# Optimization experiments

Hardware: AMD Instinct MI355X
Metric: run time of the kernel (lower is better)

The kernel has to match this reference:

```python
import jax, jax.numpy as jnp
import numpy as np
from jax import lax

# Static model/config sizes
B, ANG, C, H, NF, NB = 1, 9, 3, 128, 16, 2


def get_freq_position(n):
    """Anti-diagonal frequency bands of an n x n angular-DCT grid (python/static)."""
    bands = []
    for i in range(n):
        bands.append(([i], [0]))
    for j in range(1, n):
        bands.append(([n - 1], [j]))
    for item in bands:
        while item[0][0] > 0 and item[1][0] < n - 1:
            item[0].insert(0, item[0][0] - 1)
            item[1].insert(0, item[1][0] + 1)
    return bands


def dct_mat(n):
    """Orthonormal DCT-II matrix (row k = k-th basis)."""
    k = jnp.arange(n, dtype=jnp.float32)[:, None]
    i = jnp.arange(n, dtype=jnp.float32)[None, :]
    m = jnp.cos(jnp.pi * (i + 0.5) * k / n) * jnp.sqrt(2.0 / n)
    return m.at[0].multiply(1.0 / np.sqrt(2.0))


def conv3d(x, w, b):
    # x: (N, Cin, D, H, W), w: (Cout, Cin, 3, 3, 3)
    y = lax.conv_general_dilated(x, w, (1, 1, 1), 'SAME',
                                 dimension_numbers=('NCDHW', 'OIDHW', 'NCDHW'))
    return y + b[None, :, None, None, None]


def branch(cut, wi, bi, a, wb, bb):
    """init conv + NB ResBlock3D (PReLU -> Conv3d, residual), plus outer skip."""
    y0 = conv3d(cut, wi, bi)
    y = y0
    for k in range(NB):
        r = jnp.where(y >= 0, y, a[k] * y)  # PReLU (single-parameter)
        y = y + conv3d(r, wb[k], bb[k])
    return y0 + y


def setup_inputs() -> dict:
    key = jax.random.key(0)
    ks = jax.random.split(key, 32)

    def nrm(k, shape, s=0.05):
        return jax.random.normal(k, shape, dtype=jnp.float32) * s

    inp = {"x": jax.random.normal(ks[0], (B, ANG, ANG, C, H, H), dtype=jnp.float32)}
    i = 1
    for n in ("dc", "lo", "mi", "hi"):
        inp[f"w_{n}_i"] = nrm(ks[i], (NF, C, 3, 3, 3)); i += 1
        inp[f"b_{n}_i"] = nrm(ks[i], (NF,)); i += 1
        inp[f"a_{n}"] = jnp.full((NB,), 0.25, dtype=jnp.float32)
        inp[f"w_{n}"] = nrm(ks[i], (NB, NF, NF, 3, 3, 3)); i += 1
        inp[f"b_{n}"] = nrm(ks[i], (NB, NF)); i += 1
    inp["w_last"] = nrm(ks[i], (C, NF))  # 1x1 Conv2d, no bias
    return inp


def reference(x, w_dc_i, b_dc_i, a_dc, w_dc, b_dc,
              w_lo_i, b_lo_i, a_lo, w_lo, b_lo,
              w_mi_i, b_mi_i, a_mi, w_mi, b_mi,
              w_hi_i, b_hi_i, a_hi, w_hi, b_hi, w_last):
    b, u, v, c, h, w = x.shape
    Da = dct_mat(u)  # angular DCT (u == v)
    Ds = dct_mat(h)  # spatial DCT (h == w)

    # SpaAngDCT: spatial 2D DCT then angular 2D DCT
    xf = jnp.einsum('buvchw,Hh,Ww->buvcHW', x, Ds, Ds)
    xf = jnp.einsum('buvchw,Uu,Vv->bUVchw', xf, Da, Da)

    x_rec = jnp.zeros((b, NF, u, v, h, w), dtype=x.dtype)
    for idx, (ui, vi) in enumerate(get_freq_position(u)):
        if idx == 0:
            p = (w_dc_i, b_dc_i, a_dc, w_dc, b_dc)
        elif idx <= 2:
            p = (w_lo_i, b_lo_i, a_lo, w_lo, b_lo)
        elif idx <= u - 1:
            p = (w_mi_i, b_mi_i, a_mi, w_mi, b_mi)
        else:
            p = (w_hi_i, b_hi_i, a_hi, w_hi, b_hi)
        ua, va = jnp.array(ui), jnp.array(vi)
        cut = xf[:, ua, va].transpose(0, 2, 1, 3, 4)  # (b, c, L, h, w)
        out = branch(cut, *p)                          # (b, NF, L, h, w)
        x_rec = x_rec.at[:, :, ua, va].set(out)        # scatter band back

    # 'b c u v h w -> b c (u h) (v w)' then 1x1 conv (NF -> 3)
    xr = x_rec.transpose(0, 1, 2, 4, 3, 5).reshape(b, NF, u * h, v * w)
    xr = jnp.einsum('bnHW,on->boHW', xr, w_last)
    xr = xr.reshape(b, c, u, h, v, w).transpose(0, 2, 4, 1, 3, 5)  # (b,u,v,c,h,w)

    # InverseSpaAngDCT: angular IDCT then spatial IDCT
    xr = jnp.einsum('bUVchw,Uu,Vv->buvchw', xr, Da, Da)
    xr = jnp.einsum('buvcHW,Hh,Ww->buvchw', xr, Ds, Ds)
    return xr + x
```

## Files before the change

### kernel.cpp

```cpp
#include <hip/hip_runtime.h>
#include <hip/hip_bf16.h>
#include <math.h>

typedef __hip_bfloat16 bf16;
typedef __attribute__((ext_vector_type(8))) short short8;
typedef __attribute__((ext_vector_type(4))) float floatx4;
typedef __attribute__((ext_vector_type(4))) unsigned int uint4v;
typedef __attribute__((ext_vector_type(2))) unsigned int uint2v;

#define HW 16384
#define NSLICE 243

__constant__ int c_s_of_p[81] = {
  0, 1,1, 2,2,2, 3,3,3,3, 4,4,4,4,4, 5,5,5,5,5,5, 6,6,6,6,6,6,6,
  7,7,7,7,7,7,7,7, 8,8,8,8,8,8,8,8,8, 9,9,9,9,9,9,9,9,
  10,10,10,10,10,10,10, 11,11,11,11,11,11, 12,12,12,12,12,
  13,13,13,13, 14,14,14, 15,15, 16};
__constant__ int c_l_of_p[81] = {
  0, 0,1, 0,1,2, 0,1,2,3, 0,1,2,3,4, 0,1,2,3,4,5, 0,1,2,3,4,5,6,
  0,1,2,3,4,5,6,7, 0,1,2,3,4,5,6,7,8, 0,1,2,3,4,5,6,7,
  0,1,2,3,4,5,6, 0,1,2,3,4,5, 0,1,2,3,4, 0,1,2,3, 0,1,2, 0,1, 0};
__constant__ int c_L_of_s[17] = {1,2,3,4,5,6,7,8,9,8,7,6,5,4,3,2,1};
__constant__ int c_g_of_s[17] = {0,1,1,2,2,2,2,2,2,3,3,3,3,3,3,3,3};
__constant__ int c_pos_uv[81] = {
  0,1,3,6,10,15,21,28,36,
  2,4,7,11,16,22,29,37,45,
  5,8,12,17,23,30,38,46,53,
  9,13,18,24,31,39,47,54,60,
  14,19,25,32,40,48,55,61,66,
  20,26,33,41,49,56,62,67,71,
  27,34,42,50,57,63,68,72,75,
  35,43,51,58,64,69,73,76,78,
  44,52,59,65,70,74,77,79,80};

struct WPtrs {
  const float* wi[4]; const float* bi[4]; const float* a[4];
  const float* wb[4]; const float* bb[4]; const float* wl;
};

__device__ __forceinline__ unsigned short f2bf(float f) {
  return __bfloat16_as_ushort(__float2bfloat16(f));
}
__device__ __forceinline__ float bflo(unsigned int w) {
  return __uint_as_float(w << 16);
}
__device__ __forceinline__ float bfhi(unsigned int w) {
  return __uint_as_float(w & 0xffff0000u);
}
__device__ __forceinline__ unsigned int pack2(float a, float b) {
  return (unsigned int)f2bf(a) | ((unsigned int)f2bf(b) << 16);
}
__device__ __forceinline__ float invprelu(float v, float invA) {
  return (v >= 0.f) ? v : v * invA;
}
__device__ __forceinline__ void bfsplit(float v, unsigned short& hi, unsigned short& lo) {
  unsigned int bits = __float_as_uint(v);
  hi = (unsigned short)(bits >> 16);
  lo = f2bf(v - __uint_as_float(bits & 0xffff0000u));
}

__global__ __launch_bounds__(256) void k_setup(float* DaF,
                                               unsigned short* TFhi, unsigned short* TFlo,
                                               unsigned short* TIhi, unsigned short* TIlo) {
  const double PI = 3.14159265358979323846;
  int t = blockIdx.x * 256 + threadIdx.x;
  if (t < 81) {
    int U = t / 9, u = t % 9;
    double d = cos(PI * (u + 0.5) * U / 9.0) * sqrt(2.0 / 9.0);
    if (U == 0) d *= (1.0 / sqrt(2.0));
    DaF[t] = (float)d;
  }
  if (t < 16384) {
    int jj = t & 7, lane = (t >> 3) & 63, ks = (t >> 9) & 3, tile = t >> 11;
    int row = tile * 16 + (lane & 15);
    int colk = ks * 32 + (lane >> 4) * 8 + jj;
    double vF = cos(PI * (colk + 0.5) * row / 128.0) * sqrt(2.0 / 128.0);
    if (row == 0) vF *= (1.0 / sqrt(2.0));
    double vI = cos(PI * (row + 0.5) * colk / 128.0) * sqrt(2.0 / 128.0);
    if (colk == 0) vI *= (1.0 / sqrt(2.0));
    unsigned short h, l;
    bfsplit((float)vF, h, l); TFhi[t] = h; TFlo[t] = l;
    bfsplit((float)vI, h, l); TIhi[t] = h; TIlo[t] = l;
  }
}

__global__ __launch_bounds__(256) void k_prep(WPtrs P, unsigned short* Wmf,
                                              float* BiF, float* BbF,
                                              float* AF, float* WlF) {
  int t = blockIdx.x * 256 + threadIdx.x;
  if (t < 92160) {
    int s = t / 7680, r = t % 7680;
    int step = r / 512, r2 = r % 512;
    int lane = r2 >> 3, j = r2 & 7;
    int d = step / 5, i = step % 5;
    int q = lane >> 4, m = lane & 15;
    int tl = 2 * i + (q >> 1);
    int cin = (q & 1) * 8 + j;
    float val = 0.f;
    if (tl <= 8) {
      int ky = tl / 3, kx = tl % 3;
      int tap = d * 9 + ky * 3 + kx;
      if (s < 4) {
        if (cin < 3) val = P.wi[s][(m * 3 + cin) * 27 + tap];
      } else {
        int g = (s - 4) >> 1, k = (s - 4) & 1;
        val = P.wb[g][((k * 16 + m) * 16 + cin) * 27 + tap];
      }
    }
    Wmf[t] = f2bf(val);
  }
  if (t < 64)  BiF[t] = P.bi[t / 16][t % 16];
  if (t < 128) BbF[t] = P.bb[t / 32][t % 32];
  if (t < 8)   AF[t]  = P.a[t / 2][t % 2];
  if (t < 48)  WlF[t] = P.wl[t];
}

__global__ __launch_bounds__(256) void k_dct2(const float* __restrict__ X,
                                              const unsigned short* __restrict__ tabhi,
                                              const unsigned short* __restrict__ tablo,
                                              const float* __restrict__ xres,
                                              float* __restrict__ Y) {
  __shared__ unsigned short sThi[128 * 136];
  __shared__ unsigned short sTlo[128 * 136];
  int s = blockIdx.x;
  int t = threadIdx.x;
  int lane = t & 63, wv = t >> 6;
  int q = lane >> 4, n16 = lane & 15;
  const float* Xs = X + (size_t)s * HW;

  floatx4 acc[2][8];
#pragma unroll
  for (int mt = 0; mt < 2; mt++)
#pragma unroll
    for (int nt = 0; nt < 8; nt++) acc[mt][nt] = (floatx4){0.f, 0.f, 0.f, 0.f};

#pragma unroll
  for (int ks = 0; ks < 4; ks++) {
    short8 ahi[2], alo[2];
#pragma unroll
    for (int mt = 0; mt < 2; mt++) {
      const float* xp = Xs + (wv * 32 + mt * 16 + n16) * 128 + ks * 32 + q * 8;
      float4 a = *(const float4*)xp;
      float4 b = *(const float4*)(xp + 4);
      union { short8 v; unsigned short u[8]; } H, L;
      float xv[8] = {a.x, a.y, a.z, a.w, b.x, b.y, b.z, b.w};
#pragma unroll
      for (int j = 0; j < 8; j++) bfsplit(xv[j], H.u[j], L.u[j]);
      ahi[mt] = H.v; alo[mt] = L.v;
    }
#pragma unroll
    for (int nt = 0; nt < 8; nt++) {
      int e = nt * 2048 + ks * 512 + lane * 8;
      short8 bh = *(const short8*)(tabhi + e);
      short8 bl = *(const short8*)(tablo + e);
#pragma unroll
      for (int mt = 0; mt < 2; mt++) {
        acc[mt][nt] = __builtin_amdgcn_mfma_f32_16x16x32_bf16(ahi[mt], bl, acc[mt][nt], 0, 0, 0);
        acc[mt][nt] = __builtin_amdgcn_mfma_f32_16x16x32_bf16(alo[mt], bh, acc[mt][nt], 0, 0, 0);
        acc[mt][nt] = __builtin_amdgcn_mfma_f32_16x16x32_bf16(ahi[mt], bh, acc[mt][nt], 0, 0, 0);
      }
    }
  }

#pragma unroll
  for (int mt = 0; mt < 2; mt++)
#pragma unroll
    for (int nt = 0; nt < 8; nt++) {
      int col = nt * 16 + n16;
      int rowb = wv * 32 + mt * 16 + q * 4;
#pragma unroll
      for (int rp = 0; rp < 4; rp += 2) {
        unsigned short h0, l0, h1, l1;
        bfsplit(acc[mt][nt][rp], h0, l0);
        bfsplit(acc[mt][nt][rp + 1], h1, l1);
        int widx = (col * 136 + rowb + rp) >> 1;
        ((unsigned int*)sThi)[widx] = (unsigned int)h0 | ((unsigned int)h1 << 16);
        ((unsigned int*)sTlo)[widx] = (unsigned int)l0 | ((unsigned int)l1 << 16);
      }
    }
  __syncthreads();

#pragma unroll
  for (int mt = 0; mt < 2; mt++)
#pragma unroll
    for (int nt = 0; nt < 8; nt++) acc[mt][nt] = (floatx4){0.f, 0.f, 0.f, 0.f};

#pragma unroll
  for (int ks = 0; ks < 4; ks++) {
    short8 ahi[2], alo[2];
#pragma unroll
    for (int mt = 0; mt < 2; mt++) {
      int e = (wv * 2 + mt) * 2048 + ks * 512 + lane * 8;
      ahi[mt] = *(const short8*)(tabhi + e);
      alo[mt] = *(const short8*)(tablo + e);
    }
#pragma unroll
    for (int nt = 0; nt < 8; nt++) {
      int off = (nt * 16 + n16) * 136 + ks * 32 + q * 8;
      short8 bh = *(const short8*)(sThi + off);
      short8 bl = *(const short8*)(sTlo + off);
#pragma unroll
      for (int mt = 0; mt < 2; mt++) {
        acc[mt][nt] = __builtin_amdgcn_mfma_f32_16x16x32_bf16(ahi[mt], bl, acc[mt][nt], 0, 0, 0);
        acc[mt][nt] = __builtin_amdgcn_mfma_f32_16x16x32_bf16(alo[mt], bh, acc[mt][nt], 0, 0, 0);
        acc[mt][nt] = __builtin_amdgcn_mfma_f32_16x16x32_bf16(ahi[mt], bh, acc[mt][nt], 0, 0, 0);
      }
    }
  }

#pragma unroll
  for (int mt = 0; mt < 2; mt++)
#pragma unroll
    for (int nt = 0; nt < 8; nt++) {
      int row0 = wv * 32 + mt * 16 + q * 4;
      int col = nt * 16 + n16;
#pragma unroll
      for (int r = 0; r < 4; r++) {
        size_t oi = (size_t)s * HW + (size_t)(row0 + r) * 128 + col;
        float v = acc[mt][nt][r];
        if (xres) v += xres[oi];
        Y[oi] = v;
      }
    }
}

__global__ __launch_bounds__(256) void k_angu(const float* __restrict__ in,
                                              const float* __restrict__ DaF,
                                              float* __restrict__ out) {
  __shared__ float sDa[81];
  int t = threadIdx.x;
  if (t < 81) sDa[t] = DaF[t];
  __syncthreads();
  int idx = blockIdx.x * 256 + t;
  int hw = idx & (HW - 1);
  int r = idx >> 14;
  int c = r % 3, v = r / 3;
  float f[9];
#pragma unroll
  for (int u = 0; u < 9; u++) f[u] = in[(size_t)((u * 9 + v) * 3 + c) * HW + hw];
#pragma unroll
  for (int U = 0; U < 9; U++) {
    float acc = 0.f;
#pragma unroll
    for (int u = 0; u < 9; u++) acc += sDa[U * 9 + u] * f[u];
    out[(size_t)((U * 9 + v) * 3 + c) * HW + hw] = acc;
  }
}

__global__ __launch_bounds__(256) void k_angv(const float* __restrict__ in,
                                              const float* __restrict__ DaF,
                                              unsigned short* __restrict__ xf2b) {
  __shared__ float sDa[81];
  int t = threadIdx.x;
  if (t < 81) sDa[t] = DaF[t];
  __syncthreads();
  int idx = blockIdx.x * 256 + t;
  int hw = idx & (HW - 1);
  int r = idx >> 14;
  int c = r % 3, U = r / 3;
  float f[9];
#pragma unroll
  for (int v = 0; v < 9; v++) f[v] = in[(size_t)((U * 9 + v) * 3 + c) * HW + hw];
#pragma unroll
  for (int V = 0; V < 9; V++) {
    float acc = 0.f;
#pragma unroll
    for (int v = 0; v < 9; v++) acc += sDa[V * 9 + v] * f[v];
    size_t base = ((size_t)c_pos_uv[U * 9 + V] * HW + hw) * 4;
    xf2b[base + c] = f2bf(acc);
    if (c == 0) xf2b[base + 3] = 0;
  }
}

__global__ __launch_bounds__(256) void k_angvi(const float* __restrict__ xrb,
                                               const float* __restrict__ DaF,
                                               float* __restrict__ out) {
  __shared__ float sDa[81];
  int t = threadIdx.x;
  if (t < 81) sDa[t] = DaF[t];
  __syncthreads();
  int idx = blockIdx.x * 256 + t;
  int hw = idx & (HW - 1);
  int r = idx >> 14;
  int c = r % 3, U = r / 3;
  float f[9];
#pragma unroll
  for (int V = 0; V < 9; V++)
    f[V] = xrb[((size_t)c_pos_uv[U * 9 + V] * 3 + c) * HW + hw];
#pragma unroll
  for (int v = 0; v < 9; v++) {
    float acc = 0.f;
#pragma unroll
    for (int V = 0; V < 9; V++) acc += sDa[V * 9 + v] * f[V];
    out[(size_t)((U * 9 + v) * 3 + c) * HW + hw] = acc;
  }
}

__global__ __launch_bounds__(256) void k_angui(const float* __restrict__ in,
                                               const float* __restrict__ DaF,
                                               float* __restrict__ out) {
  __shared__ float sDa[81];
  int t = threadIdx.x;
  if (t < 81) sDa[t] = DaF[t];
  __syncthreads();
  int idx = blockIdx.x * 256 + t;
  int hw = idx & (HW - 1);
  int r = idx >> 14;
  int c = r % 3, v = r / 3;
  float f[9];
#pragma unroll
  for (int U = 0; U < 9; U++) f[U] = in[(size_t)((U * 9 + v) * 3 + c) * HW + hw];
#pragma unroll
  for (int u = 0; u < 9; u++) {
    float acc = 0.f;
#pragma unroll
    for (int U = 0; U < 9; U++) acc += sDa[U * 9 + u] * f[U];
    out[(size_t)((u * 9 + v) * 3 + c) * HW + hw] = acc;
  }
}

__global__ __launch_bounds__(256) void k_conv(const unsigned short* __restrict__ src,
                                              const unsigned short* __restrict__ prevAct,
                                              const unsigned short* __restrict__ Wmf,
                                              const float* __restrict__ BiF,
                                              const float* __restrict__ BbF,
                                              const float* __restrict__ AF,
                                              int sel,
                                              unsigned short* __restrict__ bout) {
  __shared__ unsigned short s_lds[12672];
  int p = blockIdx.y;
  int s = c_s_of_p[p], l = c_l_of_p[p];
  int g = c_g_of_s[s], Ls = c_L_of_s[s];
  int row0 = blockIdx.x * 4;
  int t = threadIdx.x;
  int lane = t & 63, wv = t >> 6;
  int q = lane >> 4, n = lane & 15;

  float aNext = (sel < 2) ? AF[g * 2 + sel] : 0.f;
  float invA  = (sel > 0) ? 1.0f / AF[g * 2 + sel - 1] : 0.f;

  int basel = wv * 4224 + (q & 1) * 2112 + n * 16;
  int off2[5];
#pragma unroll
  for (int i = 0; i < 5; i++) {
    int tl = 2 * i + (q >> 1);
    if (tl > 8) tl = 8;
    int ky = tl / 3, kx = tl % 3;
    off2[i] = basel + ky * 4224 + kx * 16;
  }

  int setIdx = (sel == 0) ? g : (4 + g * 2 + (sel - 1));
  const char* WsetBase = (const char*)Wmf + (size_t)setIdx * 15 * 1024;

  floatx4 acc[8];
#pragma unroll
  for (int cg = 0; cg < 8; cg++) acc[cg] = (floatx4){0.f, 0.f, 0.f, 0.f};

  for (int d = 0; d < 3; d++) {
    int l2 = l + d - 1;
    if (l2 < 0 || l2 >= Ls) continue;
    int p2 = p + d - 1;
    __syncthreads();
    for (int c = t; c < 1560; c += 256) {
      int half = c & 1, cc = c >> 1;
      int col = cc % 130, row = cc / 130;
      int grow = row0 - 1 + row, gcol = col - 1;
      bool v = ((unsigned)grow < 128u) && ((unsigned)gcol < 128u);
      uint4v val = (uint4v){0u, 0u, 0u, 0u};
      if (sel == 0) {
        if (v && half == 0) {
          const unsigned int* sp = (const unsigned int*)(src) +
              ((size_t)p2 * HW + grow * 128 + gcol) * 2;
          val.x = sp[0]; val.y = sp[1];
        }
      } else {
        if (v) {
          val = *(const uint4v*)(src +
              (((size_t)p2 * HW + grow * 128 + gcol) * 16 + half * 8));
        }
      }
      *(uint4v*)((char*)s_lds + ((size_t)((row * 2 + half) * 132 + col)) * 16) = val;
    }
    __syncthreads();
    short8 af[5];
#pragma unroll
    for (int i = 0; i < 5; i++)
      af[i] = *(const short8*)(WsetBase + ((d * 5 + i) * 64 + lane) * 16);
#pragma unroll
    for (int cg = 0; cg < 8; cg++) {
#pragma unroll
      for (int i = 0; i < 5; i++) {
        short8 b = *(const short8*)((const char*)s_lds + off2[i] + cg * 256);
        acc[cg] = __builtin_amdgcn_mfma_f32_16x16x32_bf16(af[i], b, acc[cg], 0, 0, 0);
      }
    }
  }

  const float* bp = (sel == 0) ? (BiF + g * 16) : (BbF + g * 32 + (sel - 1) * 16);
  float bz[4];
#pragma unroll
  for (int r = 0; r < 4; r++) bz[r] = bp[q * 4 + r];
  int h = row0 + wv;
#pragma unroll
  for (int cg = 0; cg < 8; cg++) {
    size_t pix = (size_t)p * HW + h * 128 + cg * 16 + n;
    float r0 = acc[cg][0] + bz[0], r1 = acc[cg][1] + bz[1];
    float r2 = acc[cg][2] + bz[2], r3 = acc[cg][3] + bz[3];
    if (sel != 0) {
      uint2v pv = *(const uint2v*)(prevAct + pix * 16 + q * 4);
      r0 += invprelu(bflo(pv.x), invA); r1 += invprelu(bfhi(pv.x), invA);
      r2 += invprelu(bflo(pv.y), invA); r3 += invprelu(bfhi(pv.y), invA);
    }
    if (sel < 2) {
      r0 = fmaxf(r0, 0.f) + aNext * fminf(r0, 0.f);
      r1 = fmaxf(r1, 0.f) + aNext * fminf(r1, 0.f);
      r2 = fmaxf(r2, 0.f) + aNext * fminf(r2, 0.f);
      r3 = fmaxf(r3, 0.f) + aNext * fminf(r3, 0.f);
    }
    uint2v ov; ov.x = pack2(r0, r1); ov.y = pack2(r2, r3);
    *(uint2v*)(bout + pix * 16 + q * 4) = ov;
  }
}

__global__ __launch_bounds__(256) void k_epi(const unsigned short* __restrict__ b0,
                                             const unsigned short* __restrict__ b2,
                                             const float* __restrict__ WlF,
                                             const float* __restrict__ AF,
                                             float* __restrict__ xrb) {
  int idx = blockIdx.x * 256 + threadIdx.x;
  int hw = idx & (HW - 1);
  int p = idx >> 14;
  int g = c_g_of_s[c_s_of_p[p]];
  float invA0 = 1.0f / AF[g * 2];
  size_t base = ((size_t)p * HW + hw) * 16;
  uint4v a0 = *(const uint4v*)(b0 + base);
  uint4v a1 = *(const uint4v*)(b0 + base + 8);
  uint4v c0 = *(const uint4v*)(b2 + base);
  uint4v c1 = *(const uint4v*)(b2 + base + 8);
  float v[16];
  v[0]  = invprelu(bflo(a0.x), invA0) + bflo(c0.x);
  v[1]  = invprelu(bfhi(a0.x), invA0) + bfhi(c0.x);
  v[2]  = invprelu(bflo(a0.y), invA0) + bflo(c0.y);
  v[3]  = invprelu(bfhi(a0.y), invA0) + bfhi(c0.y);
  v[4]  = invprelu(bflo(a0.z), invA0) + bflo(c0.z);
  v[5]  = invprelu(bfhi(a0.z), invA0) + bfhi(c0.z);
  v[6]  = invprelu(bflo(a0.w), invA0) + bflo(c0.w);
  v[7]  = invprelu(bfhi(a0.w), invA0) + bfhi(c0.w);
  v[8]  = invprelu(bflo(a1.x), invA0) + bflo(c1.x);
  v[9]  = invprelu(bfhi(a1.x), invA0) + bfhi(c1.x);
  v[10] = invprelu(bflo(a1.y), invA0) + bflo(c1.y);
  v[11] = invprelu(bfhi(a1.y), invA0) + bfhi(c1.y);
  v[12] = invprelu(bflo(a1.z), invA0) + bflo(c1.z);
  v[13] = invprelu(bfhi(a1.z), invA0) + bfhi(c1.z);
  v[14] = invprelu(bflo(a1.w), invA0) + bflo(c1.w);
  v[15] = invprelu(bfhi(a1.w), invA0) + bfhi(c1.w);
  float o0 = 0.f, o1 = 0.f, o2 = 0.f;
#pragma unroll
  for (int k = 0; k < 16; k++) {
    o0 += WlF[k] * v[k]; o1 += WlF[16 + k] * v[k]; o2 += WlF[32 + k] * v[k];
  }
  xrb[((size_t)p * 3 + 0) * HW + hw] = o0;
  xrb[((size_t)p * 3 + 1) * HW + hw] = o1;
  xrb[((size_t)p * 3 + 2) * HW + hw] = o2;
}

extern "C" void kernel_launch(void* const* d_in, const int* in_sizes, int n_in,
                              void* d_out, int out_size, void* d_ws, size_t ws_size,
                              hipStream_t stream) {
  (void)in_sizes; (void)n_in; (void)out_size; (void)ws_size;
  const float* x = (const float*)d_in[0];
  WPtrs P;
  for (int g = 0; g < 4; g++) {
    int b = 1 + g * 5;
    P.wi[g] = (const float*)d_in[b + 0];
    P.bi[g] = (const float*)d_in[b + 1];
    P.a[g]  = (const float*)d_in[b + 2];
    P.wb[g] = (const float*)d_in[b + 3];
    P.bb[g] = (const float*)d_in[b + 4];
  }
  P.wl = (const float*)d_in[21];

  char* base = (char*)d_ws;
  size_t off = 0;
  auto take = [&](size_t bytes) -> char* {
    char* r = base + off;
    off += (bytes + 255) & ~(size_t)255;
    return r;
  };
  float* DaF = (float*)take(81 * 4);
  unsigned short* TFhi = (unsigned short*)take(16384 * 2);
  unsigned short* TFlo = (unsigned short*)take(16384 * 2);
  unsigned short* TIhi = (unsigned short*)take(16384 * 2);
  unsigned short* TIlo = (unsigned short*)take(16384 * 2);
  unsigned short* Wmf = (unsigned short*)take(92160 * 2);
  float* BiF   = (float*)take(256);
  float* BbF   = (float*)take(512);
  float* AF    = (float*)take(32);
  float* WlF   = (float*)take(192);
  float* R1 = (float*)take((size_t)NSLICE * HW * 4);
  float* R2 = (float*)take((size_t)NSLICE * HW * 4);
  float* R3 = (float*)take((size_t)NSLICE * HW * 4);
  unsigned short* braw0 = (unsigned short*)take((size_t)81 * 16 * HW * 2);
  unsigned short* braw1 = (unsigned short*)take((size_t)81 * 16 * HW * 2);
  unsigned short* braw2 = (unsigned short*)take((size_t)81 * 16 * HW * 2);
  unsigned short* xf2b = (unsigned short*)R3;
  float* xrb = R3;

  k_setup<<<64, 256, 0, stream>>>(DaF, TFhi, TFlo, TIhi, TIlo);
  k_prep<<<360, 256, 0, stream>>>(P, Wmf, BiF, BbF, AF, WlF);
  k_dct2<<<243, 256, 0, stream>>>(x, TFhi, TFlo, nullptr, R1);
  k_angu<<<1728, 256, 0, stream>>>(R1, DaF, R2);
  k_angv<<<1728, 256, 0, stream>>>(R2, DaF, xf2b);
  k_conv<<<dim3(32, 81), 256, 0, stream>>>(xf2b, nullptr, Wmf, BiF, BbF, AF, 0, braw0);
  k_conv<<<dim3(32, 81), 256, 0, stream>>>(braw0, braw0, Wmf, BiF, BbF, AF, 1, braw1);
  k_conv<<<dim3(32, 81), 256, 0, stream>>>(braw1, braw1, Wmf, BiF, BbF, AF, 2, braw2);
  k_epi<<<5184, 256, 0, stream>>>(braw0, braw2, WlF, AF, xrb);
  k_angvi<<<1728, 256, 0, stream>>>(xrb, DaF, R2);
  k_angui<<<1728, 256, 0, stream>>>(R2, DaF, R1);
  k_dct2<<<243, 256, 0, stream>>>(R1, TIhi, TIlo, x, (float*)d_out);
}
```

Before: 317.3 us.

## Fuse epilogue 1x1 conv into last conv pass and enlarge conv tiles

The final ResBlock conv pass now does the outer skip addition and the 16-to-3 channel 1x1 projection in its epilogue, using a cross-lane shuffle reduction, and writes xrb directly. This removes the separate k_epi kernel and one full bf16 activation buffer round trip. Conv blocks also grow to 512 threads covering 8 rows, with a simpler staging loop: halo and padding LDS cells are zeroed once up front and each thread loads fixed columns, with no per-element div/mod. The cost is more LDS per block and fewer blocks in the grid.

```diff
diff --git a/kernel.cpp b/kernel.cpp
--- a/kernel.cpp
+++ b/kernel.cpp
@@ -319,25 +319,43 @@
   }
 }
 
-__global__ __launch_bounds__(256) void k_conv(const unsigned short* __restrict__ src,
+__global__ __launch_bounds__(512) void k_conv(const unsigned short* __restrict__ src,
                                               const unsigned short* __restrict__ prevAct,
+                                              const unsigned short* __restrict__ act0,
                                               const unsigned short* __restrict__ Wmf,
                                               const float* __restrict__ BiF,
                                               const float* __restrict__ BbF,
                                               const float* __restrict__ AF,
+                                              const float* __restrict__ WlF,
                                               int sel,
-                                              unsigned short* __restrict__ bout) {
-  __shared__ unsigned short s_lds[12672];
+                                              unsigned short* __restrict__ boutAct,
+                                              float* __restrict__ xrbOut) {
+  __shared__ unsigned short s_lds[10 * 132 * 16];
   int p = blockIdx.y;
   int s = c_s_of_p[p], l = c_l_of_p[p];
   int g = c_g_of_s[s], Ls = c_L_of_s[s];
-  int row0 = blockIdx.x * 4;
+  int row0 = blockIdx.x * 8;
   int t = threadIdx.x;
   int lane = t & 63, wv = t >> 6;
   int q = lane >> 4, n = lane & 15;
 
   float aNext = (sel < 2) ? AF[g * 2 + sel] : 0.f;
   float invA  = (sel > 0) ? 1.0f / AF[g * 2 + sel - 1] : 0.f;
+
+  int scol = t & 127;
+  int shalf = (t >> 7) & 1;
+  int srow0 = t >> 8;
+
+  {
+    uint4v z = (uint4v){0u, 0u, 0u, 0u};
+    int zmax = (sel == 0) ? 1320 : 40;
+    for (int i = t; i < zmax; i += 512) {
+      int row, half, col;
+      if (i < 40) { row = i >> 2; half = (i >> 1) & 1; col = (i & 1) ? 129 : 0; }
+      else { int j = i - 40; row = j >> 7; col = (j & 127) + 1; half = 1; }
+      *(uint4v*)((char*)s_lds + (size_t)(((row * 2 + half) * 132 + col)) * 16) = z;
+    }
+  }
 
   int basel = wv * 4224 + (q & 1) * 2112 + n * 16;
   int off2[5];
@@ -361,25 +379,30 @@
     if (l2 < 0 || l2 >= Ls) continue;
     int p2 = p + d - 1;
     __syncthreads();
-    for (int c = t; c < 1560; c += 256) {
-      int half = c & 1, cc = c >> 1;
-      int col = cc % 130, row = cc / 130;
-      int grow = row0 - 1 + row, gcol = col - 1;
-      bool v = ((unsigned)grow < 128u) && ((unsigned)gcol < 128u);
-      uint4v val = (uint4v){0u, 0u, 0u, 0u};
-      if (sel == 0) {
-        if (v && half == 0) {
-          const unsigned int* sp = (const unsigned int*)(src) +
-              ((size_t)p2 * HW + grow * 128 + gcol) * 2;
-          val.x = sp[0]; val.y = sp[1];
+    if (sel == 0) {
+      if (shalf == 0) {
+#pragma unroll
+        for (int it = 0; it < 5; it++) {
+          int row = srow0 + it * 2;
+          int grow = row0 - 1 + row;
+          uint2v v2 = (uint2v){0u, 0u};
+          if ((unsigned)grow < 128u)
+            v2 = *(const uint2v*)(src + ((size_t)p2 * HW + grow * 128 + scol) * 4);
+          uint4v val; val.x = v2.x; val.y = v2.y; val.z = 0u; val.w = 0u;
+          *(uint4v*)((char*)s_lds + (size_t)((row * 2) * 132 + scol + 1) * 16) = val;
         }
-      } else {
-        if (v) {
+      }
+    } else {
+#pragma unroll
+      for (int it = 0; it < 5; it++) {
+        int row = srow0 + it * 2;
+        int grow = row0 - 1 + row;
+        uint4v val = (uint4v){0u, 0u, 0u, 0u};
+        if ((unsigned)grow < 128u)
           val = *(const uint4v*)(src +
-              (((size_t)p2 * HW + grow * 128 + gcol) * 16 + half * 8));
-        }
-      }
-      *(uint4v*)((char*)s_lds + ((size_t)((row * 2 + half) * 132 + col)) * 16) = val;
+              (((size_t)p2 * HW + grow * 128 + scol) * 16 + shalf * 8));
+        *(uint4v*)((char*)s_lds + (size_t)((row * 2 + shalf) * 132 + scol + 1) * 16) = val;
+      }
     }
     __syncthreads();
     short8 af[5];
@@ -401,67 +424,59 @@
 #pragma unroll
   for (int r = 0; r < 4; r++) bz[r] = bp[q * 4 + r];
   int h = row0 + wv;
-#pragma unroll
-  for (int cg = 0; cg < 8; cg++) {
-    size_t pix = (size_t)p * HW + h * 128 + cg * 16 + n;
-    float r0 = acc[cg][0] + bz[0], r1 = acc[cg][1] + bz[1];
-    float r2 = acc[cg][2] + bz[2], r3 = acc[cg][3] + bz[3];
-    if (sel != 0) {
-      uint2v pv = *(const uint2v*)(prevAct + pix * 16 + q * 4);
-      r0 += invprelu(bflo(pv.x), invA); r1 += invprelu(bfhi(pv.x), invA);
-      r2 += invprelu(bflo(pv.y), invA); r3 += invprelu(bfhi(pv.y), invA);
-    }
-    if (sel < 2) {
+
+  if (sel < 2) {
+#pragma unroll
+    for (int cg = 0; cg < 8; cg++) {
+      size_t pix = (size_t)p * HW + h * 128 + cg * 16 + n;
+      float r0 = acc[cg][0] + bz[0], r1 = acc[cg][1] + bz[1];
+      float r2 = acc[cg][2] + bz[2], r3 = acc[cg][3] + bz[3];
+      if (sel != 0) {
+        uint2v pv = *(const uint2v*)(prevAct + pix * 16 + q * 4);
+        r0 += invprelu(bflo(pv.x), invA); r1 += invprelu(bfhi(pv.x), invA);
+        r2 += invprelu(bflo(pv.y), invA); r3 += invprelu(bfhi(pv.y), invA);
+      }
       r0 = fmaxf(r0, 0.f) + aNext * fminf(r0, 0.f);
       r1 = fmaxf(r1, 0.f) + aNext * fminf(r1, 0.f);
       r2 = fmaxf(r2, 0.f) + aNext * fminf(r2, 0.f);
       r3 = fmaxf(r3, 0.f) + aNext * fminf(r3, 0.f);
-    }
-    uint2v ov; ov.x = pack2(r0, r1); ov.y = pack2(r2, r3);
-    *(uint2v*)(bout + pix * 16 + q * 4) = ov;
-  }
-}
-
-__global__ __launch_bounds__(256) void k_epi(const unsigned short* __restrict__ b0,
-                                             const unsigned short* __restrict__ b2,
-                                             const float* __restrict__ WlF,
-                                             const float* __restrict__ AF,
-                                             float* __restrict__ xrb) {
-  int idx = blockIdx.x * 256 + threadIdx.x;
-  int hw = idx & (HW - 1);
-  int p = idx >> 14;
-  int g = c_g_of_s[c_s_of_p[p]];
-  float invA0 = 1.0f / AF[g * 2];
-  size_t base = ((size_t)p * HW + hw) * 16;
-  uint4v a0 = *(const uint4v*)(b0 + base);
-  uint4v a1 = *(const uint4v*)(b0 + base + 8);
-  uint4v c0 = *(const uint4v*)(b2 + base);
-  uint4v c1 = *(const uint4v*)(b2 + base + 8);
-  float v[16];
-  v[0]  = invprelu(bflo(a0.x), invA0) + bflo(c0.x);
-  v[1]  = invprelu(bfhi(a0.x), invA0) + bfhi(c0.x);
-  v[2]  = invprelu(bflo(a0.y), invA0) + bflo(c0.y);
-  v[3]  = invprelu(bfhi(a0.y), invA0) + bfhi(c0.y);
-  v[4]  = invprelu(bflo(a0.z), invA0) + bflo(c0.z);
-  v[5]  = invprelu(bfhi(a0.z), invA0) + bfhi(c0.z);
-  v[6]  = invprelu(bflo(a0.w), invA0) + bflo(c0.w);
-  v[7]  = invprelu(bfhi(a0.w), invA0) + bfhi(c0.w);
-  v[8]  = invprelu(bflo(a1.x), invA0) + bflo(c1.x);
-  v[9]  = invprelu(bfhi(a1.x), invA0) + bfhi(c1.x);
-  v[10] = invprelu(bflo(a1.y), invA0) + bflo(c1.y);
-  v[11] = invprelu(bfhi(a1.y), invA0) + bfhi(c1.y);
-  v[12] = invprelu(bflo(a1.z), invA0) + bflo(c1.z);
-  v[13] = invprelu(bfhi(a1.z), invA0) + bfhi(c1.z);
-  v[14] = invprelu(bflo(a1.w), invA0) + bflo(c1.w);
-  v[15] = invprelu(bfhi(a1.w), invA0) + bfhi(c1.w);
-  float o0 = 0.f, o1 = 0.f, o2 = 0.f;
-#pragma unroll
-  for (int k = 0; k < 16; k++) {
-    o0 += WlF[k] * v[k]; o1 += WlF[16 + k] * v[k]; o2 += WlF[32 + k] * v[k];
-  }
-  xrb[((size_t)p * 3 + 0) * HW + hw] = o0;
-  xrb[((size_t)p * 3 + 1) * HW + hw] = o1;
-  xrb[((size_t)p * 3 + 2) * HW + hw] = o2;
+      uint2v ov; ov.x = pack2(r0, r1); ov.y = pack2(r2, r3);
+      *(uint2v*)(boutAct + pix * 16 + q * 4) = ov;
+    }
+  } else {
+    float invA0 = 1.0f / AF[g * 2];
+    float wl0[4], wl1[4], wl2[4];
+#pragma unroll
+    for (int r = 0; r < 4; r++) {
+      wl0[r] = WlF[q * 4 + r];
+      wl1[r] = WlF[16 + q * 4 + r];
+      wl2[r] = WlF[32 + q * 4 + r];
+    }
+#pragma unroll
+    for (int cg = 0; cg < 8; cg++) {
+      size_t pix = (size_t)p * HW + h * 128 + cg * 16 + n;
+      float r0 = acc[cg][0] + bz[0], r1 = acc[cg][1] + bz[1];
+      float r2 = acc[cg][2] + bz[2], r3 = acc[cg][3] + bz[3];
+      uint2v pv = *(const uint2v*)(prevAct + pix * 16 + q * 4);
+      r0 += invprelu(bflo(pv.x), invA); r1 += invprelu(bfhi(pv.x), invA);
+      r2 += invprelu(bflo(pv.y), invA); r3 += invprelu(bfhi(pv.y), invA);
+      uint2v p0 = *(const uint2v*)(act0 + pix * 16 + q * 4);
+      r0 += invprelu(bflo(p0.x), invA0); r1 += invprelu(bfhi(p0.x), invA0);
+      r2 += invprelu(bflo(p0.y), invA0); r3 += invprelu(bfhi(p0.y), invA0);
+      float o0 = wl0[0] * r0 + wl0[1] * r1 + wl0[2] * r2 + wl0[3] * r3;
+      float o1 = wl1[0] * r0 + wl1[1] * r1 + wl1[2] * r2 + wl1[3] * r3;
+      float o2 = wl2[0] * r0 + wl2[1] * r1 + wl2[2] * r2 + wl2[3] * r3;
+      o0 += __shfl_xor(o0, 16); o0 += __shfl_xor(o0, 32);
+      o1 += __shfl_xor(o1, 16); o1 += __shfl_xor(o1, 32);
+      o2 += __shfl_xor(o2, 16); o2 += __shfl_xor(o2, 32);
+      if (q == 0) {
+        size_t hw = (size_t)h * 128 + cg * 16 + n;
+        xrbOut[((size_t)p * 3 + 0) * HW + hw] = o0;
+        xrbOut[((size_t)p * 3 + 1) * HW + hw] = o1;
+        xrbOut[((size_t)p * 3 + 2) * HW + hw] = o2;
+      }
+    }
+  }
 }
 
 extern "C" void kernel_launch(void* const* d_in, const int* in_sizes, int n_in,
@@ -502,7 +517,6 @@
   float* R3 = (float*)take((size_t)NSLICE * HW * 4);
   unsigned short* braw0 = (unsigned short*)take((size_t)81 * 16 * HW * 2);
   unsigned short* braw1 = (unsigned short*)take((size_t)81 * 16 * HW * 2);
-  unsigned short* braw2 = (unsigned short*)take((size_t)81 * 16 * HW * 2);
   unsigned short* xf2b = (unsigned short*)R3;
   float* xrb = R3;
 
@@ -511,10 +525,12 @@
   k_dct2<<<243, 256, 0, stream>>>(x, TFhi, TFlo, nullptr, R1);
   k_angu<<<1728, 256, 0, stream>>>(R1, DaF, R2);
   k_angv<<<1728, 256, 0, stream>>>(R2, DaF, xf2b);
-  k_conv<<<dim3(32, 81), 256, 0, stream>>>(xf2b, nullptr, Wmf, BiF, BbF, AF, 0, braw0);
-  k_conv<<<dim3(32, 81), 256, 0, stream>>>(braw0, braw0, Wmf, BiF, BbF, AF, 1, braw1);
-  k_conv<<<dim3(32, 81), 256, 0, stream>>>(braw1, braw1, Wmf, BiF, BbF, AF, 2, braw2);
-  k_epi<<<5184, 256, 0, stream>>>(braw0, braw2, WlF, AF, xrb);
+  k_conv<<<dim3(16, 81), 512, 0, stream>>>(xf2b, nullptr, nullptr, Wmf,
+                                           BiF, BbF, AF, WlF, 0, braw0, nullptr);
+  k_conv<<<dim3(16, 81), 512, 0, stream>>>(braw0, braw0, nullptr, Wmf,
+                                           BiF, BbF, AF, WlF, 1, braw1, nullptr);
+  k_conv<<<dim3(16, 81), 512, 0, stream>>>(braw1, braw1, braw0, Wmf,
+                                           BiF, BbF, AF, WlF, 2, nullptr, xrb);
   k_angvi<<<1728, 256, 0, stream>>>(xrb, DaF, R2);
   k_angui<<<1728, 256, 0, stream>>>(R2, DaF, R1);
   k_dct2<<<243, 256, 0, stream>>>(R1, TIhi, TIlo, x, (float*)d_out);
```

Measured after the change: 299.3 us. -5.7%, faster.
